# Optimization experiments

Hardware: AMD Instinct MI355X
Metric: run time of the kernel (lower is better)

## Reference

```python
import jax, jax.numpy as jnp
import numpy as np

EXP_SCALE = 10.0   # self.exp_param_scale
BETA_UP = 5.0      # self.kernel_beta_upbound
N_HEAD = 12


def setup_inputs() -> dict:
    key = jax.random.key(0)
    ks = jax.random.split(key, 7)
    B, T, C, nh = 2, 2048, 768, N_HEAD
    s = 1.0 / np.sqrt(C)
    x = jax.random.normal(ks[0], (B, T, C), jnp.float32)
    W_la = jax.random.normal(ks[1], (C, C), jnp.float32) * s      # LeakyAverage linear
    la_coef = jax.random.uniform(ks[2], (nh,), jnp.float32)        # per-head leaky decay in (0,1)
    W_v = jax.random.normal(ks[3], (C, C), jnp.float32) * s        # v_featurizer linear
    v_coef = jax.random.uniform(ks[4], (nh,), jnp.float32)         # v_featurizer per-head coef
    kernel_beta = jnp.ones((nh,), jnp.float32) / EXP_SCALE
    value_beta = jnp.ones((nh,), jnp.float32) * (-0.5 / EXP_SCALE)
    W_proj = jax.random.normal(ks[5], (C, C), jnp.float32) * s     # c_proj
    return dict(x=x, W_la=W_la, la_coef=la_coef, W_v=W_v, v_coef=v_coef,
                kernel_beta=kernel_beta, value_beta=value_beta, W_proj=W_proj)


def _leaky_average(x, W_la, la_coef):
    # y_t = c * y_{t-1} + (1-c) * (x W^T)_t, per-head decay c. Returns (B, nh, T, hs).
    B, T, C = x.shape
    nh = la_coef.shape[0]
    hs = C // nh
    u = (x @ W_la.T).reshape(B, T, nh, hs)
    c = la_coef[None, :, None]  # (1, nh, 1) broadcast over (B, nh, hs)

    def step(carry, ut):
        y = c * carry + (1.0 - c) * ut
        return y, y

    _, ys = jax.lax.scan(step, jnp.zeros((B, nh, hs), x.dtype), jnp.swapaxes(u, 0, 1))
    return jnp.transpose(ys, (1, 2, 0, 3))  # (T,B,nh,hs) -> (B,nh,T,hs)


def reference(x, W_la, la_coef, W_v, v_coef, kernel_beta, value_beta, W_proj):
    B, T, C = x.shape
    nh = la_coef.shape[0]
    hs = C // nh
    v_shift = 1

    # K path: leaky-average features, L2-normalize, exp-kernel beta scale
    k0 = _leaky_average(x, W_la, la_coef)                               # (B,nh,T,hs)
    raw_k = k0 / (jnp.linalg.norm(k0, axis=-1, keepdims=True) + 1e-6)
    beta = jnp.exp(jnp.minimum(kernel_beta * EXP_SCALE, BETA_UP))
    k = raw_k * beta[None, :, None, None]

    # V path: lowrlinearconv featurizer (linear, shift-by-1 mix, normalize) + value scale
    xl = (x @ W_v.T).reshape(B, T, nh, hs).transpose(0, 2, 1, 3)        # (B,nh,T,hs)
    shifted = jnp.concatenate([xl[:, :, 1:], jnp.zeros_like(xl[:, :, :1])], axis=2)
    vc = v_coef[None, :, None, None]
    vf = shifted * (1.0 - vc) + xl * vc
    vf = vf / (jnp.linalg.norm(vf, axis=-1, keepdims=True) + 1e-6)
    vbeta = jnp.exp(jnp.minimum(value_beta * EXP_SCALE, BETA_UP))
    v = vf * vbeta[None, :, None, None]

    # shifted-causal attention: query at position t (t>=1) attends keys 0..t-1, scale=1.0
    q = k[:, :, v_shift:]                                               # (B,nh,T-1,hs)
    scores = jnp.einsum('bhqd,bhkd->bhqk', q, k)                        # (B,nh,T-1,T)
    mask = jnp.tril(jnp.ones((T - v_shift, T), bool))                   # j <= iq  <=>  key < query pos
    scores = jnp.where(mask, scores, -jnp.inf)
    attn = jax.nn.softmax(scores, axis=-1)
    o = jnp.einsum('bhqk,bhkd->bhqd', attn, v)
    y = jnp.concatenate([jnp.zeros((B, nh, v_shift, hs), x.dtype), o], axis=2)

    y = y.transpose(0, 2, 1, 3).reshape(B, T, C)
    return y @ W_proj.T  # c_proj (dropouts are identity in eval)
```

## Files before the change

kernel.cpp:

```cpp
#include <hip/hip_runtime.h>
#include <hip/hip_bf16.h>
#include <math.h>

#define B_   2
#define T_   2048
#define C_   768
#define NH   12
#define HS   64
#define NSEG 64
#define SEGLEN 32
#define CX   1536

typedef __attribute__((ext_vector_type(8))) short short8;
typedef __attribute__((ext_vector_type(4))) short short4v;
typedef __attribute__((ext_vector_type(4))) float f32x4;

static __device__ inline unsigned short f2b(float f) {
  __hip_bfloat16 h = __float2bfloat16(f);
  unsigned short u;
  __builtin_memcpy(&u, &h, 2);
  return u;
}
static __device__ inline float b2f(unsigned short u) {
  unsigned int x = ((unsigned int)u) << 16;
  float f;
  __builtin_memcpy(&f, &x, 4);
  return f;
}

#define GLOAD_LDS16(gp, lp)                                                        \
  __builtin_amdgcn_global_load_lds((const __attribute__((address_space(1))) void*)(gp), \
                                   (__attribute__((address_space(3))) void*)(lp), 16, 0, 0)

__global__ __launch_bounds__(256) void cast_all(const float* __restrict__ x,
                                                const float* __restrict__ wla,
                                                const float* __restrict__ wv,
                                                const float* __restrict__ wp,
                                                __hip_bfloat16* __restrict__ xb,
                                                __hip_bfloat16* __restrict__ wcat,
                                                __hip_bfloat16* __restrict__ wpb) {
  const int NX4 = (B_ * T_ * C_) / 4;
  const int NW4 = (C_ * C_) / 4;
  const int TOT = NX4 + 3 * NW4;
  int i = blockIdx.x * 256 + threadIdx.x;
  int st = gridDim.x * 256;
  for (; i < TOT; i += st) {
    const float* s;
    unsigned short* d;
    if (i < NX4) { s = x + (size_t)i * 4; d = (unsigned short*)xb + (size_t)i * 4; }
    else if (i < NX4 + NW4) { int j = i - NX4; s = wla + (size_t)j * 4; d = (unsigned short*)wcat + (size_t)j * 4; }
    else if (i < NX4 + 2 * NW4) { int j = i - NX4 - NW4; s = wv + (size_t)j * 4; d = (unsigned short*)wcat + (size_t)(C_ * C_) + (size_t)j * 4; }
    else { int j = i - NX4 - 2 * NW4; s = wp + (size_t)j * 4; d = (unsigned short*)wpb + (size_t)j * 4; }
    float4 v = *(const float4*)s;
    short4v o;
    o.x = (short)f2b(v.x); o.y = (short)f2b(v.y); o.z = (short)f2b(v.z); o.w = (short)f2b(v.w);
    *(short4v*)d = o;
  }
}

template <int BM, bool OB16>
__global__ __launch_bounds__(256) void gemm_bf16(const __hip_bfloat16* __restrict__ A,
                                                 const __hip_bfloat16* __restrict__ Bw,
                                                 void* __restrict__ Cv,
                                                 int M, int N, int K) {
  __shared__ __hip_bfloat16 As[BM * 64];
  __shared__ __hip_bfloat16 Bs[128 * 64];
  const int tid = threadIdx.x;
  const int w = tid >> 6, lane = tid & 63;
  const int bm = blockIdx.x * BM, bn = blockIdx.y * 128;
  const int q16 = lane & 15, lg = lane >> 4;

  constexpr int NACC = (BM == 128) ? 4 : 2;
  f32x4 acc[4][NACC];
#pragma unroll
  for (int i = 0; i < 4; ++i)
#pragma unroll
    for (int j = 0; j < NACC; ++j) acc[i][j] = (f32x4){0.f, 0.f, 0.f, 0.f};

  const int srow = (lane >> 3);
  const int soff0 = (lane & 7) * 16;
  const int sw = (lane & 7) << 4;
  constexpr int ACH = BM / 8;
  constexpr int CPW = (ACH + 16) / 4;

  for (int k0 = 0; k0 < K; k0 += 64) {
    __syncthreads();
#pragma unroll
    for (int c = 0; c < CPW; ++c) {
      int gc = w * CPW + c;
      int isB = gc >= ACH;
      int ci = isB ? gc - ACH : gc;
      int row = ci * 8 + srow;
      int soff = soff0 ^ ((row & 7) << 4);
      const __hip_bfloat16* gp =
          (isB ? Bw + (size_t)(bn + row) * K : A + (size_t)(bm + row) * K) + k0 + (soff >> 1);
      __hip_bfloat16* lp = (isB ? Bs : As) + ci * 512;
      GLOAD_LDS16(gp, lp);
    }
    __syncthreads();
#pragma unroll
    for (int ks = 0; ks < 2; ++ks) {
      short8 af[4], bf[NACC];
      const int colb = ks * 64 + lg * 16;
#pragma unroll
      for (int i = 0; i < 4; ++i) {
        int ra = (BM == 128) ? ((w >> 1) * 64 + i * 16 + q16) : (i * 16 + q16);
        af[i] = *(const short8*)((const char*)As + ra * 128 + (colb ^ sw));
      }
#pragma unroll
      for (int j = 0; j < NACC; ++j) {
        int rb = (BM == 128) ? ((w & 1) * 64 + j * 16 + q16) : (w * 32 + j * 16 + q16);
        bf[j] = *(const short8*)((const char*)Bs + rb * 128 + (colb ^ sw));
      }
#pragma unroll
      for (int i = 0; i < 4; ++i)
#pragma unroll
        for (int j = 0; j < NACC; ++j)
          acc[i][j] = __builtin_amdgcn_mfma_f32_16x16x32_bf16(af[i], bf[j], acc[i][j], 0, 0, 0);
    }
  }
#pragma unroll
  for (int i = 0; i < 4; ++i) {
#pragma unroll
    for (int r = 0; r < 4; ++r) {
      int m = (BM == 128) ? (bm + (w >> 1) * 64 + i * 16 + lg * 4 + r)
                          : (bm + i * 16 + lg * 4 + r);
      int nb = (BM == 128) ? (bn + (w & 1) * 64 + q16) : (bn + w * 32 + q16);
      if (OB16) {
        unsigned short* cp = (unsigned short*)Cv + (size_t)m * N + nb;
#pragma unroll
        for (int j = 0; j < NACC; ++j) cp[j * 16] = f2b(acc[i][j][r]);
      } else {
        float* cp = (float*)Cv + (size_t)m * N + nb;
#pragma unroll
        for (int j = 0; j < NACC; ++j) cp[j * 16] = acc[i][j][r];
      }
    }
  }
}

__global__ __launch_bounds__(256) void scan_seg(const unsigned short* __restrict__ uxv,
                                                const float* __restrict__ la_coef,
                                                float* __restrict__ segend) {
  int cid = blockIdx.x * 4 + (threadIdx.x >> 6);
  int d   = threadIdx.x & 63;
  int seg = cid & (NSEG - 1);
  int bh  = cid >> 6;
  int h   = bh % NH;
  int b   = bh / NH;
  float c  = la_coef[h];
  float oc = 1.f - c;
  int t0 = seg * SEGLEN;
  const unsigned short* up = uxv + ((size_t)b * T_ + t0) * CX + h * HS + d;
  float uv[SEGLEN];
#pragma unroll
  for (int i = 0; i < SEGLEN; ++i) uv[i] = b2f(up[(size_t)i * CX]);
  float y = 0.f;
#pragma unroll
  for (int i = 0; i < SEGLEN; ++i) y = fmaf(c, y, oc * uv[i]);
  segend[(size_t)cid * HS + d] = y;
}

__global__ __launch_bounds__(256) void scan_b(const float* __restrict__ la_coef,
                                              const float* __restrict__ segend,
                                              float* __restrict__ carryin) {
  int s = blockIdx.x * 256 + threadIdx.x;
  if (s >= B_ * NH * HS) return;
  int d  = s & 63;
  int bh = s >> 6;
  int h  = bh % NH;
  float c = la_coef[h];
  float cl = c;
#pragma unroll
  for (int i = 0; i < 5; ++i) cl *= cl;
  float h0 = 0.f;
  for (int seg = 0; seg < NSEG; ++seg) {
    int cid = bh * NSEG + seg;
    carryin[(size_t)cid * HS + d] = h0;
    h0 = fmaf(cl, h0, segend[(size_t)cid * HS + d]);
  }
}

__global__ __launch_bounds__(256) void scanc_vbuild(const float* __restrict__ la_coef,
                                                    const float* __restrict__ kernel_beta,
                                                    const float* __restrict__ carryin,
                                                    const unsigned short* __restrict__ uxv,
                                                    const float* __restrict__ v_coef,
                                                    const float* __restrict__ value_beta,
                                                    __hip_bfloat16* __restrict__ kb16,
                                                    __hip_bfloat16* __restrict__ vt) {
  __shared__ __hip_bfloat16 sm[64][73];
  const int NBC = B_ * NH * NSEG / 4;
  if ((int)blockIdx.x < NBC) {
    int cid = blockIdx.x * 4 + (threadIdx.x >> 6);
    int d   = threadIdx.x & 63;
    int seg = cid & (NSEG - 1);
    int bh  = cid >> 6;
    int h   = bh % NH;
    int b   = bh / NH;
    float c  = la_coef[h];
    float oc = 1.f - c;
    float bk = __expf(fminf(kernel_beta[h] * 10.f, 5.f));
    int t0 = seg * SEGLEN;
    const unsigned short* up = uxv + ((size_t)b * T_ + t0) * CX + h * HS + d;
    __hip_bfloat16* op = kb16 + ((size_t)bh * T_ + t0) * HS + d;
    float uv[SEGLEN];
#pragma unroll
    for (int i = 0; i < SEGLEN; ++i) uv[i] = b2f(up[(size_t)i * CX]);
    float y = carryin[(size_t)cid * HS + d];
    for (int i = 0; i < SEGLEN; ++i) {
      y = fmaf(c, y, oc * uv[i]);
      float ss = y * y;
#pragma unroll
      for (int off = 1; off < 64; off <<= 1) ss += __shfl_xor(ss, off, 64);
      float scale = bk / (sqrtf(ss) + 1e-6f);
      op[(size_t)i * HS] = __float2bfloat16(y * scale);
    }
  } else {
    int idx = blockIdx.x - NBC;
    int t0 = (idx & 31) * 64;
    int bh = idx >> 5;
    int h = bh % NH, b = bh / NH;
    int w = threadIdx.x >> 6, lane = threadIdx.x & 63;
    float vc = v_coef[h];
    float vb = __expf(fminf(value_beta[h] * 10.f, 5.f));
    for (int i = 0; i < 16; ++i) {
      int tl = w * 16 + i;
      int t = t0 + tl;
      const unsigned short* xp = uxv + ((size_t)b * T_ + t) * CX + 768 + h * HS + lane;
      float x0 = b2f(*xp);
      float x1 = (t + 1 < T_) ? b2f(xp[CX]) : 0.f;
      float vf = (1.f - vc) * x1 + vc * x0;
      float ss = vf * vf;
#pragma unroll
      for (int off = 1; off < 64; off <<= 1) ss += __shfl_xor(ss, off, 64);
      sm[tl][lane] = __float2bfloat16(vf * vb / (sqrtf(ss) + 1e-6f));
    }
    __syncthreads();
    int d = threadIdx.x >> 3;
    int c = threadIdx.x & 7;
    for (int i = 0; i < 2; ++i) {
      int dd = d + i * 32;
      short8 v;
#pragma unroll
      for (int k = 0; k < 8; ++k)
        v[k] = (short)((const unsigned short*)&sm[c * 8 + k][dd])[0];
      *(short8*)((unsigned short*)vt + ((size_t)bh * HS + dd) * T_ + t0 + c * 8) = v;
    }
  }
}

__global__ __launch_bounds__(256, 4) void attn7(const __hip_bfloat16* __restrict__ Kg,
                                                const __hip_bfloat16* __restrict__ Vtg,
                                                const float* __restrict__ kernel_beta,
                                                __hip_bfloat16* __restrict__ Y) {
  __shared__ __hip_bfloat16 Kt[2][64 * 64];
  __shared__ __hip_bfloat16 Vt[3][64 * 64];
  __shared__ char Pl[4][2304];
  const int bh = blockIdx.x;
  const int b = bh / NH, h = bh % NH;
  const int w = threadIdx.x >> 6, lane = threadIdx.x & 63;
  const int q16 = lane & 15, lg = lane >> 4;
  const int it = 31 - blockIdx.y;
  const int qb0 = 1 + it * 64;
  float bk = __expf(fminf(kernel_beta[h] * 10.f, 5.f));
  const float L2E = 1.4426950408889634f;
  float m0l = bk * bk * L2E;
  const unsigned short* Kh = (const unsigned short*)Kg + (size_t)bh * T_ * HS;
  const unsigned short* Vh = (const unsigned short*)Vtg + (size_t)bh * HS * T_;
  unsigned short* Yh = (unsigned short*)Y + (size_t)b * T_ * C_ + h * HS;

  if (it == 0 && w == 0) Yh[lane] = 0;

  const int tq = qb0 + w * 16 + q16;
  short8 qf[2];
  {
    int tqc = tq > T_ - 1 ? T_ - 1 : tq;
#pragma unroll
    for (int ks = 0; ks < 2; ++ks)
      qf[ks] = *(const short8*)(Kh + (size_t)tqc * HS + ks * 32 + lg * 8);
  }

  f32x4 zero = {0.f, 0.f, 0.f, 0.f};
  f32x4 accO[4];
#pragma unroll
  for (int mt = 0; mt < 4; ++mt) accO[mt] = zero;
  float lsum = 0.f;
  f32x4 sp[4];

  char* pb = &Pl[w][0] + q16 * 144;
  const int swr = (q16 & 7) << 4;

  const int srow = lane >> 3;
  const int soff = ((lane & 7) << 4) ^ (srow << 4);

  const int NT = (qb0 + 126) >> 6;

#define STAGE_KV(kbuf, vbuf, j0)                                                      \
  {                                                                                   \
    _Pragma("unroll")                                                                 \
    for (int n = 0; n < 2; ++n) {                                                     \
      int ch = w * 2 + n;                                                             \
      int row = ch * 8 + srow;                                                        \
      GLOAD_LDS16((const char*)(Kh + (size_t)((j0) + row) * HS) + soff,               \
                  &Kt[kbuf][ch * 512]);                                               \
      GLOAD_LDS16((const char*)(Vh + (size_t)row * T_ + (j0)) + soff,                 \
                  &Vt[vbuf][ch * 512]);                                               \
    }                                                                                 \
  }

#define SM_PV(tp)                                                                     \
  {                                                                                   \
    const int j0p = (tp)*64;                                                          \
    const char* Vb = (const char*)&Vt[(tp) % 3][0];                                   \
    _Pragma("unroll")                                                                 \
    for (int nt = 0; nt < 4; ++nt) {                                                  \
      float p[4];                                                                     \
      _Pragma("unroll")                                                               \
      for (int r = 0; r < 4; ++r) {                                                   \
        int j = j0p + nt * 16 + lg * 4 + r;                                           \
        p[r] = (j < tq) ? exp2f(fmaf(sp[nt][r], L2E, -m0l)) : 0.f;                    \
        lsum += p[r];                                                                 \
      }                                                                               \
      unsigned int w0, w1;                                                            \
      asm("v_cvt_pk_bf16_f32 %0, %1, %2" : "=v"(w0) : "v"(p[0]), "v"(p[1]));          \
      asm("v_cvt_pk_bf16_f32 %0, %1, %2" : "=v"(w1) : "v"(p[2]), "v"(p[3]));          \
      uint2 pk; pk.x = w0; pk.y = w1;                                                 \
      *(uint2*)(pb + nt * 32 + lg * 8) = pk;                                          \
    }                                                                                 \
    __builtin_amdgcn_s_setprio(1);                                                    \
    _Pragma("unroll")                                                                 \
    for (int ks = 0; ks < 2; ++ks) {                                                  \
      short8 pf = *(const short8*)(pb + ks * 64 + lg * 16);                           \
      _Pragma("unroll")                                                               \
      for (int mt = 0; mt < 4; ++mt) {                                                \
        short8 vf = *(const short8*)(Vb + (mt * 16 + q16) * 128 +                     \
                                     ((ks * 64 + lg * 16) ^ swr));                    \
        accO[mt] = __builtin_amdgcn_mfma_f32_16x16x32_bf16(vf, pf, accO[mt], 0, 0, 0);\
      }                                                                               \
    }                                                                                 \
    __builtin_amdgcn_s_setprio(0);                                                    \
  }

  STAGE_KV(0, 0, 0);

  for (int kt = 0; kt < NT; ++kt) {
    const int j0 = kt * 64;
    if (kt + 1 < NT) {
      STAGE_KV((kt + 1) & 1, (kt + 1) % 3, j0 + 64);
      asm volatile("s_waitcnt vmcnt(4)" ::: "memory");
    } else {
      asm volatile("s_waitcnt vmcnt(0)" ::: "memory");
    }
    __builtin_amdgcn_s_barrier();
    __builtin_amdgcn_sched_barrier(0);

    const char* Kb = (const char*)&Kt[kt & 1][0];
    short8 kf[4][2];
#pragma unroll
    for (int nt = 0; nt < 4; ++nt)
#pragma unroll
      for (int ks = 0; ks < 2; ++ks)
        kf[nt][ks] = *(const short8*)(Kb + (nt * 16 + q16) * 128 + ((ks * 64 + lg * 16) ^ swr));
    f32x4 sc[4];
    __builtin_amdgcn_s_setprio(1);
#pragma unroll
    for (int nt = 0; nt < 4; ++nt) {
      sc[nt] = __builtin_amdgcn_mfma_f32_16x16x32_bf16(kf[nt][0], qf[0], zero, 0, 0, 0);
      sc[nt] = __builtin_amdgcn_mfma_f32_16x16x32_bf16(kf[nt][1], qf[1], sc[nt], 0, 0, 0);
    }
    __builtin_amdgcn_s_setprio(0);

    if (kt > 0) SM_PV(kt - 1);

#pragma unroll
    for (int nt = 0; nt < 4; ++nt) sp[nt] = sc[nt];

    asm volatile("s_waitcnt lgkmcnt(0)" ::: "memory");
    __builtin_amdgcn_s_barrier();
  }
  SM_PV(NT - 1);

  {
    float v = lsum;
    v += __shfl_xor(v, 16, 64);
    v += __shfl_xor(v, 32, 64);
    float inv = 1.f / v;
    if (tq < T_) {
      unsigned short* yp = Yh + (size_t)tq * C_;
#pragma unroll
      for (int mt = 0; mt < 4; ++mt) {
        float o0 = accO[mt][0] * inv, o1 = accO[mt][1] * inv;
        float o2 = accO[mt][2] * inv, o3 = accO[mt][3] * inv;
        unsigned int u0, u1;
        asm("v_cvt_pk_bf16_f32 %0, %1, %2" : "=v"(u0) : "v"(o0), "v"(o1));
        asm("v_cvt_pk_bf16_f32 %0, %1, %2" : "=v"(u1) : "v"(o2), "v"(o3));
        uint2 pk; pk.x = u0; pk.y = u1;
        *(uint2*)(yp + mt * 16 + lg * 4) = pk;
      }
    }
  }
#undef STAGE_KV
#undef SM_PV
}

extern "C" void kernel_launch(void* const* d_in, const int* in_sizes, int n_in,
                              void* d_out, int out_size, void* d_ws, size_t ws_size,
                              hipStream_t stream) {
  const float* x          = (const float*)d_in[0];
  const float* W_la       = (const float*)d_in[1];
  const float* la_coef    = (const float*)d_in[2];
  const float* W_v        = (const float*)d_in[3];
  const float* v_coef     = (const float*)d_in[4];
  const float* kernel_bet = (const float*)d_in[5];
  const float* value_bet  = (const float*)d_in[6];
  const float* W_proj     = (const float*)d_in[7];
  float* out = (float*)d_out;

  char* ws = (char*)d_ws;
  const size_t NTOK = (size_t)B_ * T_ * C_;
  const size_t NSEGTOT = (size_t)B_ * NH * NSEG * HS;
  unsigned short* uxv = (unsigned short*)ws;
  float* segend  = (float*)(ws + (size_t)B_ * T_ * CX * 2);
  float* carryin = segend + NSEGTOT;
  __hip_bfloat16* kb16 = (__hip_bfloat16*)(carryin + NSEGTOT);
  __hip_bfloat16* vt16 = kb16 + NTOK;
  __hip_bfloat16* xb   = vt16 + NTOK;
  __hip_bfloat16* Wcat = xb + NTOK;
  __hip_bfloat16* Wpb  = Wcat + (size_t)CX * C_;
  __hip_bfloat16* yb   = xb;

  const int M = B_ * T_;

  cast_all<<<2048, 256, 0, stream>>>(x, W_la, W_v, W_proj, xb, Wcat, Wpb);

  gemm_bf16<64, true><<<dim3(M / 64, CX / 128), 256, 0, stream>>>(xb, Wcat, uxv, M, CX, C_);

  scan_seg<<<dim3(B_ * NH * NSEG / 4), 256, 0, stream>>>(uxv, la_coef, segend);
  scan_b<<<dim3((B_ * NH * HS + 255) / 256), 256, 0, stream>>>(la_coef, segend, carryin);
  scanc_vbuild<<<dim3(B_ * NH * NSEG / 4 + 32 * B_ * NH), 256, 0, stream>>>(
      la_coef, kernel_bet, carryin, uxv, v_coef, value_bet, kb16, vt16);

  attn7<<<dim3(B_ * NH, 32), 256, 0, stream>>>(kb16, vt16, kernel_bet, yb);

  gemm_bf16<64, false><<<dim3(M / 64, C_ / 128), 256, 0, stream>>>(yb, Wpb, out, M, C_, C_);
}
```

Measured before the change: 104.4 us.

## Split attention keys across waves and fold carry scan into consumer kernel

The attention kernel now has each of the four waves handle all 64 queries of the block but only a strided quarter of the 32-key tiles. K/V fragments are loaded straight from global into registers with double buffering, and partial outputs and row sums are reduced through LDS at the end, replacing the shared-LDS staging, barriers and query-per-wave split. Separately, the scan_b kernel is removed and each segment recomputes its carry-in by serially combining the preceding segment ends. This saves a launch but adds up to 63 dependent FMAs per thread. The attention change raises register pressure (launch bounds lowered to 2) and drops LDS reuse of K/V across waves.

```diff
diff --git a/kernel.cpp b/kernel.cpp
--- a/kernel.cpp
+++ b/kernel.cpp
@@ -161,29 +161,9 @@
   segend[(size_t)cid * HS + d] = y;
 }
 
-__global__ __launch_bounds__(256) void scan_b(const float* __restrict__ la_coef,
-                                              const float* __restrict__ segend,
-                                              float* __restrict__ carryin) {
-  int s = blockIdx.x * 256 + threadIdx.x;
-  if (s >= B_ * NH * HS) return;
-  int d  = s & 63;
-  int bh = s >> 6;
-  int h  = bh % NH;
-  float c = la_coef[h];
-  float cl = c;
-#pragma unroll
-  for (int i = 0; i < 5; ++i) cl *= cl;
-  float h0 = 0.f;
-  for (int seg = 0; seg < NSEG; ++seg) {
-    int cid = bh * NSEG + seg;
-    carryin[(size_t)cid * HS + d] = h0;
-    h0 = fmaf(cl, h0, segend[(size_t)cid * HS + d]);
-  }
-}
-
 __global__ __launch_bounds__(256) void scanc_vbuild(const float* __restrict__ la_coef,
                                                     const float* __restrict__ kernel_beta,
-                                                    const float* __restrict__ carryin,
+                                                    const float* __restrict__ segend,
                                                     const unsigned short* __restrict__ uxv,
                                                     const float* __restrict__ v_coef,
                                                     const float* __restrict__ value_beta,
@@ -201,13 +181,18 @@
     float c  = la_coef[h];
     float oc = 1.f - c;
     float bk = __expf(fminf(kernel_beta[h] * 10.f, 5.f));
+    float cl = c;
+#pragma unroll
+    for (int i = 0; i < 5; ++i) cl *= cl;
+    const float* se = segend + (size_t)bh * NSEG * HS + d;
+    float y = 0.f;
+    for (int s = 0; s < seg; ++s) y = fmaf(y, cl, se[(size_t)s * HS]);
     int t0 = seg * SEGLEN;
     const unsigned short* up = uxv + ((size_t)b * T_ + t0) * CX + h * HS + d;
     __hip_bfloat16* op = kb16 + ((size_t)bh * T_ + t0) * HS + d;
     float uv[SEGLEN];
 #pragma unroll
     for (int i = 0; i < SEGLEN; ++i) uv[i] = b2f(up[(size_t)i * CX]);
-    float y = carryin[(size_t)cid * HS + d];
     for (int i = 0; i < SEGLEN; ++i) {
       y = fmaf(c, y, oc * uv[i]);
       float ss = y * y;
@@ -250,158 +235,176 @@
   }
 }
 
-__global__ __launch_bounds__(256, 4) void attn7(const __hip_bfloat16* __restrict__ Kg,
+__global__ __launch_bounds__(256, 2) void attn8(const __hip_bfloat16* __restrict__ Kg,
                                                 const __hip_bfloat16* __restrict__ Vtg,
                                                 const float* __restrict__ kernel_beta,
                                                 __hip_bfloat16* __restrict__ Y) {
-  __shared__ __hip_bfloat16 Kt[2][64 * 64];
-  __shared__ __hip_bfloat16 Vt[3][64 * 64];
-  __shared__ char Pl[4][2304];
+  __shared__ __align__(16) char lds[38912];
   const int bh = blockIdx.x;
   const int b = bh / NH, h = bh % NH;
   const int w = threadIdx.x >> 6, lane = threadIdx.x & 63;
   const int q16 = lane & 15, lg = lane >> 4;
   const int it = 31 - blockIdx.y;
   const int qb0 = 1 + it * 64;
+  const int NT32 = 2 * it + 2;
   float bk = __expf(fminf(kernel_beta[h] * 10.f, 5.f));
   const float L2E = 1.4426950408889634f;
-  float m0l = bk * bk * L2E;
+  const float m0l = bk * bk * L2E;
   const unsigned short* Kh = (const unsigned short*)Kg + (size_t)bh * T_ * HS;
   const unsigned short* Vh = (const unsigned short*)Vtg + (size_t)bh * HS * T_;
   unsigned short* Yh = (unsigned short*)Y + (size_t)b * T_ * C_ + h * HS;
 
   if (it == 0 && w == 0) Yh[lane] = 0;
 
-  const int tq = qb0 + w * 16 + q16;
-  short8 qf[2];
-  {
-    int tqc = tq > T_ - 1 ? T_ - 1 : tq;
+  short8 qf[4][2];
+#pragma unroll
+  for (int qs = 0; qs < 4; ++qs) {
+    int tqc = qb0 + qs * 16 + q16;
+    if (tqc > T_ - 1) tqc = T_ - 1;
 #pragma unroll
     for (int ks = 0; ks < 2; ++ks)
-      qf[ks] = *(const short8*)(Kh + (size_t)tqc * HS + ks * 32 + lg * 8);
+      qf[qs][ks] = *(const short8*)(Kh + (size_t)tqc * HS + ks * 32 + lg * 8);
   }
 
   f32x4 zero = {0.f, 0.f, 0.f, 0.f};
-  f32x4 accO[4];
-#pragma unroll
-  for (int mt = 0; mt < 4; ++mt) accO[mt] = zero;
-  float lsum = 0.f;
-  f32x4 sp[4];
-
-  char* pb = &Pl[w][0] + q16 * 144;
-  const int swr = (q16 & 7) << 4;
-
-  const int srow = lane >> 3;
-  const int soff = ((lane & 7) << 4) ^ (srow << 4);
-
-  const int NT = (qb0 + 126) >> 6;
-
-#define STAGE_KV(kbuf, vbuf, j0)                                                      \
+  f32x4 accO[4][4];
+#pragma unroll
+  for (int qs = 0; qs < 4; ++qs)
+#pragma unroll
+    for (int mt = 0; mt < 4; ++mt) accO[qs][mt] = zero;
+  float lsum[4] = {0.f, 0.f, 0.f, 0.f};
+  char* pwbase = lds + (size_t)w * 4 * 1152;
+
+#define LOADT(KF, VF, j0)                                                             \
   {                                                                                   \
     _Pragma("unroll")                                                                 \
-    for (int n = 0; n < 2; ++n) {                                                     \
-      int ch = w * 2 + n;                                                             \
-      int row = ch * 8 + srow;                                                        \
-      GLOAD_LDS16((const char*)(Kh + (size_t)((j0) + row) * HS) + soff,               \
-                  &Kt[kbuf][ch * 512]);                                               \
-      GLOAD_LDS16((const char*)(Vh + (size_t)row * T_ + (j0)) + soff,                 \
-                  &Vt[vbuf][ch * 512]);                                               \
-    }                                                                                 \
-  }
-
-#define SM_PV(tp)                                                                     \
+    for (int nt = 0; nt < 2; ++nt)                                                    \
+      _Pragma("unroll")                                                               \
+      for (int ks = 0; ks < 2; ++ks)                                                  \
+        KF[nt][ks] = *(const short8*)(Kh + (size_t)((j0) + nt * 16 + q16) * HS +      \
+                                      ks * 32 + lg * 8);                              \
+    _Pragma("unroll")                                                                 \
+    for (int mt = 0; mt < 4; ++mt)                                                    \
+      VF[mt] = *(const short8*)(Vh + (size_t)(mt * 16 + q16) * T_ + (j0) + lg * 8);   \
+  }
+
+#define COMPUTE(KF, VF, ktv)                                                          \
   {                                                                                   \
-    const int j0p = (tp)*64;                                                          \
-    const char* Vb = (const char*)&Vt[(tp) % 3][0];                                   \
+    const int j0c = (ktv)*32;                                                         \
     _Pragma("unroll")                                                                 \
-    for (int nt = 0; nt < 4; ++nt) {                                                  \
-      float p[4];                                                                     \
+    for (int qs = 0; qs < 4; ++qs) {                                                  \
+      const int tqq = qb0 + qs * 16 + q16;                                            \
+      char* pb = pwbase + qs * 1152 + q16 * 72;                                       \
+      f32x4 s0 = __builtin_amdgcn_mfma_f32_16x16x32_bf16(KF[0][0], qf[qs][0], zero, 0, 0, 0); \
+      s0 = __builtin_amdgcn_mfma_f32_16x16x32_bf16(KF[0][1], qf[qs][1], s0, 0, 0, 0); \
+      f32x4 s1 = __builtin_amdgcn_mfma_f32_16x16x32_bf16(KF[1][0], qf[qs][0], zero, 0, 0, 0); \
+      s1 = __builtin_amdgcn_mfma_f32_16x16x32_bf16(KF[1][1], qf[qs][1], s1, 0, 0, 0); \
+      float p0[4], p1[4];                                                             \
       _Pragma("unroll")                                                               \
       for (int r = 0; r < 4; ++r) {                                                   \
-        int j = j0p + nt * 16 + lg * 4 + r;                                           \
-        p[r] = (j < tq) ? exp2f(fmaf(sp[nt][r], L2E, -m0l)) : 0.f;                    \
-        lsum += p[r];                                                                 \
+        int j0r = j0c + lg * 4 + r;                                                   \
+        p0[r] = (j0r < tqq) ? exp2f(fmaf(s0[r], L2E, -m0l)) : 0.f;                    \
+        int j1r = j0c + 16 + lg * 4 + r;                                              \
+        p1[r] = (j1r < tqq) ? exp2f(fmaf(s1[r], L2E, -m0l)) : 0.f;                    \
+        lsum[qs] += p0[r] + p1[r];                                                    \
       }                                                                               \
-      unsigned int w0, w1;                                                            \
-      asm("v_cvt_pk_bf16_f32 %0, %1, %2" : "=v"(w0) : "v"(p[0]), "v"(p[1]));          \
-      asm("v_cvt_pk_bf16_f32 %0, %1, %2" : "=v"(w1) : "v"(p[2]), "v"(p[3]));          \
-      uint2 pk; pk.x = w0; pk.y = w1;                                                 \
-      *(uint2*)(pb + nt * 32 + lg * 8) = pk;                                          \
+      unsigned int w00, w01, w10, w11;                                                \
+      asm("v_cvt_pk_bf16_f32 %0, %1, %2" : "=v"(w00) : "v"(p0[0]), "v"(p0[1]));       \
+      asm("v_cvt_pk_bf16_f32 %0, %1, %2" : "=v"(w01) : "v"(p0[2]), "v"(p0[3]));       \
+      asm("v_cvt_pk_bf16_f32 %0, %1, %2" : "=v"(w10) : "v"(p1[0]), "v"(p1[1]));       \
+      asm("v_cvt_pk_bf16_f32 %0, %1, %2" : "=v"(w11) : "v"(p1[2]), "v"(p1[3]));       \
+      uint2 pkA; pkA.x = w00; pkA.y = w01;                                            \
+      uint2 pkB; pkB.x = w10; pkB.y = w11;                                            \
+      *(uint2*)(pb + lg * 8) = pkA;                                                   \
+      *(uint2*)(pb + 32 + lg * 8) = pkB;                                              \
+      short8 pf = *(const short8*)(pb + lg * 16);                                     \
+      _Pragma("unroll")                                                               \
+      for (int mt = 0; mt < 4; ++mt)                                                  \
+        accO[qs][mt] = __builtin_amdgcn_mfma_f32_16x16x32_bf16(VF[mt], pf, accO[qs][mt], 0, 0, 0); \
     }                                                                                 \
-    __builtin_amdgcn_s_setprio(1);                                                    \
-    _Pragma("unroll")                                                                 \
-    for (int ks = 0; ks < 2; ++ks) {                                                  \
-      short8 pf = *(const short8*)(pb + ks * 64 + lg * 16);                           \
-      _Pragma("unroll")                                                               \
-      for (int mt = 0; mt < 4; ++mt) {                                                \
-        short8 vf = *(const short8*)(Vb + (mt * 16 + q16) * 128 +                     \
-                                     ((ks * 64 + lg * 16) ^ swr));                    \
-        accO[mt] = __builtin_amdgcn_mfma_f32_16x16x32_bf16(vf, pf, accO[mt], 0, 0, 0);\
-      }                                                                               \
-    }                                                                                 \
-    __builtin_amdgcn_s_setprio(0);                                                    \
-  }
-
-  STAGE_KV(0, 0, 0);
-
-  for (int kt = 0; kt < NT; ++kt) {
-    const int j0 = kt * 64;
-    if (kt + 1 < NT) {
-      STAGE_KV((kt + 1) & 1, (kt + 1) % 3, j0 + 64);
-      asm volatile("s_waitcnt vmcnt(4)" ::: "memory");
-    } else {
-      asm volatile("s_waitcnt vmcnt(0)" ::: "memory");
-    }
-    __builtin_amdgcn_s_barrier();
-    __builtin_amdgcn_sched_barrier(0);
-
-    const char* Kb = (const char*)&Kt[kt & 1][0];
-    short8 kf[4][2];
-#pragma unroll
-    for (int nt = 0; nt < 4; ++nt)
-#pragma unroll
-      for (int ks = 0; ks < 2; ++ks)
-        kf[nt][ks] = *(const short8*)(Kb + (nt * 16 + q16) * 128 + ((ks * 64 + lg * 16) ^ swr));
-    f32x4 sc[4];
-    __builtin_amdgcn_s_setprio(1);
-#pragma unroll
-    for (int nt = 0; nt < 4; ++nt) {
-      sc[nt] = __builtin_amdgcn_mfma_f32_16x16x32_bf16(kf[nt][0], qf[0], zero, 0, 0, 0);
-      sc[nt] = __builtin_amdgcn_mfma_f32_16x16x32_bf16(kf[nt][1], qf[1], sc[nt], 0, 0, 0);
-    }
-    __builtin_amdgcn_s_setprio(0);
-
-    if (kt > 0) SM_PV(kt - 1);
-
-#pragma unroll
-    for (int nt = 0; nt < 4; ++nt) sp[nt] = sc[nt];
-
-    asm volatile("s_waitcnt lgkmcnt(0)" ::: "memory");
-    __builtin_amdgcn_s_barrier();
-  }
-  SM_PV(NT - 1);
-
-  {
-    float v = lsum;
-    v += __shfl_xor(v, 16, 64);
-    v += __shfl_xor(v, 32, 64);
-    float inv = 1.f / v;
-    if (tq < T_) {
-      unsigned short* yp = Yh + (size_t)tq * C_;
+  }
+
+  short8 kfA[2][2], vfA[4], kfB[2][2], vfB[4];
+  int kt = w;
+  if (kt < NT32) LOADT(kfA, vfA, kt * 32);
+  while (kt < NT32) {
+    if (kt + 4 < NT32) LOADT(kfB, vfB, (kt + 4) * 32);
+    COMPUTE(kfA, vfA, kt);
+    kt += 4;
+    if (kt >= NT32) break;
+    if (kt + 4 < NT32) LOADT(kfA, vfA, (kt + 4) * 32);
+    COMPUTE(kfB, vfB, kt);
+    kt += 4;
+  }
+
+  __syncthreads();
+  float* LR = (float*)(lds + 34816);
+  if (w >= 2) {
+    float* PB = (float*)(lds + (size_t)(w - 2) * 17408);
+#pragma unroll
+    for (int qs = 0; qs < 4; ++qs)
+#pragma unroll
+      for (int mt = 0; mt < 4; ++mt)
+        *(f32x4*)(PB + (qs * 16 + q16) * 68 + mt * 16 + lg * 4) = accO[qs][mt];
+  }
+#pragma unroll
+  for (int qs = 0; qs < 4; ++qs)
+    LR[((size_t)w * 64 + qs * 16 + q16) * 4 + lg] = lsum[qs];
+  __syncthreads();
+  if (w < 2) {
+    float* PB = (float*)(lds + (size_t)w * 17408);
+#pragma unroll
+    for (int qs = 0; qs < 4; ++qs)
 #pragma unroll
       for (int mt = 0; mt < 4; ++mt) {
-        float o0 = accO[mt][0] * inv, o1 = accO[mt][1] * inv;
-        float o2 = accO[mt][2] * inv, o3 = accO[mt][3] * inv;
-        unsigned int u0, u1;
-        asm("v_cvt_pk_bf16_f32 %0, %1, %2" : "=v"(u0) : "v"(o0), "v"(o1));
-        asm("v_cvt_pk_bf16_f32 %0, %1, %2" : "=v"(u1) : "v"(o2), "v"(o3));
-        uint2 pk; pk.x = u0; pk.y = u1;
-        *(uint2*)(yp + mt * 16 + lg * 4) = pk;
-      }
-    }
-  }
-#undef STAGE_KV
-#undef SM_PV
+        f32x4 o = *(f32x4*)(PB + (qs * 16 + q16) * 68 + mt * 16 + lg * 4);
+        accO[qs][mt][0] += o[0]; accO[qs][mt][1] += o[1];
+        accO[qs][mt][2] += o[2]; accO[qs][mt][3] += o[3];
+      }
+    if (w == 1) {
+#pragma unroll
+      for (int qs = 0; qs < 4; ++qs)
+#pragma unroll
+        for (int mt = 0; mt < 4; ++mt)
+          *(f32x4*)(PB + (qs * 16 + q16) * 68 + mt * 16 + lg * 4) = accO[qs][mt];
+    }
+  }
+  __syncthreads();
+  if (w == 0) {
+    float* PB1 = (float*)(lds + 17408);
+#pragma unroll
+    for (int qs = 0; qs < 4; ++qs) {
+#pragma unroll
+      for (int mt = 0; mt < 4; ++mt) {
+        f32x4 o = *(f32x4*)(PB1 + (qs * 16 + q16) * 68 + mt * 16 + lg * 4);
+        accO[qs][mt][0] += o[0]; accO[qs][mt][1] += o[1];
+        accO[qs][mt][2] += o[2]; accO[qs][mt][3] += o[3];
+      }
+      float tot = 0.f;
+#pragma unroll
+      for (int p = 0; p < 4; ++p) {
+        f32x4 lv = *(f32x4*)(LR + ((size_t)p * 64 + qs * 16 + q16) * 4);
+        tot += lv[0] + lv[1] + lv[2] + lv[3];
+      }
+      float inv = 1.f / tot;
+      int tq = qb0 + qs * 16 + q16;
+      if (tq < T_) {
+        unsigned short* yp = Yh + (size_t)tq * C_;
+#pragma unroll
+        for (int mt = 0; mt < 4; ++mt) {
+          float o0 = accO[qs][mt][0] * inv, o1 = accO[qs][mt][1] * inv;
+          float o2 = accO[qs][mt][2] * inv, o3 = accO[qs][mt][3] * inv;
+          unsigned int u0, u1;
+          asm("v_cvt_pk_bf16_f32 %0, %1, %2" : "=v"(u0) : "v"(o0), "v"(o1));
+          asm("v_cvt_pk_bf16_f32 %0, %1, %2" : "=v"(u1) : "v"(o2), "v"(o3));
+          uint2 pk; pk.x = u0; pk.y = u1;
+          *(uint2*)(yp + mt * 16 + lg * 4) = pk;
+        }
+      }
+    }
+  }
+#undef LOADT
+#undef COMPUTE
 }
 
 extern "C" void kernel_launch(void* const* d_in, const int* in_sizes, int n_in,
@@ -422,8 +425,7 @@
   const size_t NSEGTOT = (size_t)B_ * NH * NSEG * HS;
   unsigned short* uxv = (unsigned short*)ws;
   float* segend  = (float*)(ws + (size_t)B_ * T_ * CX * 2);
-  float* carryin = segend + NSEGTOT;
-  __hip_bfloat16* kb16 = (__hip_bfloat16*)(carryin + NSEGTOT);
+  __hip_bfloat16* kb16 = (__hip_bfloat16*)(segend + NSEGTOT);
   __hip_bfloat16* vt16 = kb16 + NTOK;
   __hip_bfloat16* xb   = vt16 + NTOK;
   __hip_bfloat16* Wcat = xb + NTOK;
@@ -437,11 +439,10 @@
   gemm_bf16<64, true><<<dim3(M / 64, CX / 128), 256, 0, stream>>>(xb, Wcat, uxv, M, CX, C_);
 
   scan_seg<<<dim3(B_ * NH * NSEG / 4), 256, 0, stream>>>(uxv, la_coef, segend);
-  scan_b<<<dim3((B_ * NH * HS + 255) / 256), 256, 0, stream>>>(la_coef, segend, carryin);
   scanc_vbuild<<<dim3(B_ * NH * NSEG / 4 + 32 * B_ * NH), 256, 0, stream>>>(
-      la_coef, kernel_bet, carryin, uxv, v_coef, value_bet, kb16, vt16);
-
-  attn7<<<dim3(B_ * NH, 32), 256, 0, stream>>>(kb16, vt16, kernel_bet, yb);
+      la_coef, kernel_bet, segend, uxv, v_coef, value_bet, kb16, vt16);
+
+  attn8<<<dim3(B_ * NH, 32), 256, 0, stream>>>(kb16, vt16, kernel_bet, yb);
 
   gemm_bf16<64, false><<<dim3(M / 64, C_ / 128), 256, 0, stream>>>(yb, Wpb, out, M, C_, C_);
 }
```

After: 110.3 us. +5.7%, slower.

## Rewrite attention as split-K 32x32 MFMA with paired query tiles and register P

Applied to the files above, without the earlier changes.

Replaces the attention kernel with one where each block handles two 32-row query tiles (p and 63-p) for causal load balancing. The four waves split the key range, each loading K and V tiles directly from global into registers and using 32x32x16 MFMAs. The P fragment is repacked with permlane32_swap instead of going through LDS, and partial outputs are reduced across waves through LDS at the end. Separately, the carry scan preloads segment ends into registers. The aim is to cut LDS traffic and barriers, at the cost of a cross-wave reduction and higher register pressure (launch bounds drop to 2).

```diff
diff --git a/kernel.cpp b/kernel.cpp
--- a/kernel.cpp
+++ b/kernel.cpp
@@ -14,6 +14,9 @@
 typedef __attribute__((ext_vector_type(8))) short short8;
 typedef __attribute__((ext_vector_type(4))) short short4v;
 typedef __attribute__((ext_vector_type(4))) float f32x4;
+typedef __attribute__((ext_vector_type(16))) float f32x16;
+typedef __attribute__((ext_vector_type(2))) unsigned int uint2v;
+typedef __attribute__((ext_vector_type(4))) unsigned int uint4v;
 
 static __device__ inline unsigned short f2b(float f) {
   __hip_bfloat16 h = __float2bfloat16(f);
@@ -26,6 +29,11 @@
   float f;
   __builtin_memcpy(&f, &x, 4);
   return f;
+}
+static __device__ inline unsigned cvtpk(float a, float b) {
+  unsigned r;
+  asm("v_cvt_pk_bf16_f32 %0, %1, %2" : "=v"(r) : "v"(a), "v"(b));
+  return r;
 }
 
 #define GLOAD_LDS16(gp, lp)                                                        \
@@ -173,11 +181,15 @@
   float cl = c;
 #pragma unroll
   for (int i = 0; i < 5; ++i) cl *= cl;
+  float sv[NSEG];
+#pragma unroll
+  for (int seg = 0; seg < NSEG; ++seg)
+    sv[seg] = segend[(size_t)(bh * NSEG + seg) * HS + d];
   float h0 = 0.f;
+#pragma unroll
   for (int seg = 0; seg < NSEG; ++seg) {
-    int cid = bh * NSEG + seg;
-    carryin[(size_t)cid * HS + d] = h0;
-    h0 = fmaf(cl, h0, segend[(size_t)cid * HS + d]);
+    carryin[(size_t)(bh * NSEG + seg) * HS + d] = h0;
+    h0 = fmaf(cl, h0, sv[seg]);
   }
 }
 
@@ -250,158 +262,226 @@
   }
 }
 
-__global__ __launch_bounds__(256, 4) void attn7(const __hip_bfloat16* __restrict__ Kg,
-                                                const __hip_bfloat16* __restrict__ Vtg,
-                                                const float* __restrict__ kernel_beta,
-                                                __hip_bfloat16* __restrict__ Y) {
-  __shared__ __hip_bfloat16 Kt[2][64 * 64];
-  __shared__ __hip_bfloat16 Vt[3][64 * 64];
-  __shared__ char Pl[4][2304];
+__global__ __launch_bounds__(256, 2) void attn12(const __hip_bfloat16* __restrict__ Kg,
+                                                 const __hip_bfloat16* __restrict__ Vtg,
+                                                 const float* __restrict__ kernel_beta,
+                                                 __hip_bfloat16* __restrict__ Y) {
+  __shared__ __align__(16) char lds[20992];
   const int bh = blockIdx.x;
   const int b = bh / NH, h = bh % NH;
   const int w = threadIdx.x >> 6, lane = threadIdx.x & 63;
-  const int q16 = lane & 15, lg = lane >> 4;
-  const int it = 31 - blockIdx.y;
-  const int qb0 = 1 + it * 64;
+  const int l31 = lane & 31, lg2 = lane >> 5;
+  const int p = blockIdx.y;
+  const int uA = p, uB = 63 - p;
   float bk = __expf(fminf(kernel_beta[h] * 10.f, 5.f));
   const float L2E = 1.4426950408889634f;
-  float m0l = bk * bk * L2E;
+  const float m0l = bk * bk * L2E;
   const unsigned short* Kh = (const unsigned short*)Kg + (size_t)bh * T_ * HS;
   const unsigned short* Vh = (const unsigned short*)Vtg + (size_t)bh * HS * T_;
   unsigned short* Yh = (unsigned short*)Y + (size_t)b * T_ * C_ + h * HS;
 
-  if (it == 0 && w == 0) Yh[lane] = 0;
-
-  const int tq = qb0 + w * 16 + q16;
-  short8 qf[2];
+  if (p == 0 && w == 0) Yh[lane] = 0;
+
+  short8 qfA[4], qfB[4];
   {
-    int tqc = tq > T_ - 1 ? T_ - 1 : tq;
-#pragma unroll
-    for (int ks = 0; ks < 2; ++ks)
-      qf[ks] = *(const short8*)(Kh + (size_t)tqc * HS + ks * 32 + lg * 8);
-  }
-
-  f32x4 zero = {0.f, 0.f, 0.f, 0.f};
-  f32x4 accO[4];
-#pragma unroll
-  for (int mt = 0; mt < 4; ++mt) accO[mt] = zero;
-  float lsum = 0.f;
-  f32x4 sp[4];
-
-  char* pb = &Pl[w][0] + q16 * 144;
-  const int swr = (q16 & 7) << 4;
-
-  const int srow = lane >> 3;
-  const int soff = ((lane & 7) << 4) ^ (srow << 4);
-
-  const int NT = (qb0 + 126) >> 6;
-
-#define STAGE_KV(kbuf, vbuf, j0)                                                      \
+    int ta = 1 + 32 * uA + l31; if (ta > T_ - 1) ta = T_ - 1;
+    int tb = 1 + 32 * uB + l31; if (tb > T_ - 1) tb = T_ - 1;
+#pragma unroll
+    for (int s = 0; s < 4; ++s) {
+      qfA[s] = *(const short8*)(Kh + (size_t)ta * HS + s * 16 + lg2 * 8);
+      qfB[s] = *(const short8*)(Kh + (size_t)tb * HS + s * 16 + lg2 * 8);
+    }
+  }
+
+  f32x16 zero16 = {0.f};
+  f32x16 accA[2] = {zero16, zero16}, accB[2] = {zero16, zero16};
+  float lsA = 0.f, lsB = 0.f;
+
+#define LOADT(KF, VF, j0)                                                             \
   {                                                                                   \
     _Pragma("unroll")                                                                 \
-    for (int n = 0; n < 2; ++n) {                                                     \
-      int ch = w * 2 + n;                                                             \
-      int row = ch * 8 + srow;                                                        \
-      GLOAD_LDS16((const char*)(Kh + (size_t)((j0) + row) * HS) + soff,               \
-                  &Kt[kbuf][ch * 512]);                                               \
-      GLOAD_LDS16((const char*)(Vh + (size_t)row * T_ + (j0)) + soff,                 \
-                  &Vt[vbuf][ch * 512]);                                               \
-    }                                                                                 \
-  }
-
-#define SM_PV(tp)                                                                     \
+    for (int s = 0; s < 4; ++s)                                                       \
+      KF[s] = *(const short8*)(Kh + (size_t)((j0) + l31) * HS + s * 16 + lg2 * 8);    \
+    _Pragma("unroll")                                                                 \
+    for (int ds = 0; ds < 2; ++ds)                                                    \
+      _Pragma("unroll")                                                               \
+      for (int s2 = 0; s2 < 2; ++s2)                                                  \
+        VF[ds][s2] = *(const short8*)(Vh + (size_t)(ds * 32 + l31) * T_ + (j0) +      \
+                                      s2 * 16 + lg2 * 8);                             \
+  }
+
+#define PACK_P(pq)                                                                    \
+  uint2v g00 = __builtin_amdgcn_permlane32_swap(cvtpk(pq[0], pq[1]),                  \
+                                                cvtpk(pq[4], pq[5]), false, false);   \
+  uint2v g01 = __builtin_amdgcn_permlane32_swap(cvtpk(pq[2], pq[3]),                  \
+                                                cvtpk(pq[6], pq[7]), false, false);   \
+  uint2v g10 = __builtin_amdgcn_permlane32_swap(cvtpk(pq[8], pq[9]),                  \
+                                                cvtpk(pq[12], pq[13]), false, false); \
+  uint2v g11 = __builtin_amdgcn_permlane32_swap(cvtpk(pq[10], pq[11]),                \
+                                                cvtpk(pq[14], pq[15]), false, false); \
+  uint4v pb0v, pb1v;                                                                  \
+  pb0v.x = g00.x; pb0v.y = g01.x; pb0v.z = g00.y; pb0v.w = g01.y;                     \
+  pb1v.x = g10.x; pb1v.y = g11.x; pb1v.z = g10.y; pb1v.w = g11.y;                     \
+  short8 PB0 = __builtin_bit_cast(short8, pb0v);                                      \
+  short8 PB1 = __builtin_bit_cast(short8, pb1v);
+
+#define PV_STEP(VF, ACC)                                                              \
   {                                                                                   \
-    const int j0p = (tp)*64;                                                          \
-    const char* Vb = (const char*)&Vt[(tp) % 3][0];                                   \
-    _Pragma("unroll")                                                                 \
-    for (int nt = 0; nt < 4; ++nt) {                                                  \
-      float p[4];                                                                     \
+    __builtin_amdgcn_s_setprio(1);                                                    \
+    _Pragma("unroll")                                                                 \
+    for (int ds = 0; ds < 2; ++ds) {                                                  \
+      ACC[ds] = __builtin_amdgcn_mfma_f32_32x32x16_bf16(VF[ds][0], PB0, ACC[ds], 0, 0, 0); \
+      ACC[ds] = __builtin_amdgcn_mfma_f32_32x32x16_bf16(VF[ds][1], PB1, ACC[ds], 0, 0, 0); \
+    }                                                                                 \
+    __builtin_amdgcn_s_setprio(0);                                                    \
+  }
+
+#define COMPUTE_U(KF, VF, QF, ACC, LSUM)                                              \
+  {                                                                                   \
+    f32x16 S = zero16;                                                                \
+    __builtin_amdgcn_s_setprio(1);                                                    \
+    _Pragma("unroll")                                                                 \
+    for (int s = 0; s < 4; ++s)                                                       \
+      S = __builtin_amdgcn_mfma_f32_32x32x16_bf16(KF[s], QF[s], S, 0, 0, 0);          \
+    __builtin_amdgcn_s_setprio(0);                                                    \
+    float pq[16];                                                                     \
+    _Pragma("unroll")                                                                 \
+    for (int r = 0; r < 16; ++r) {                                                    \
+      pq[r] = exp2f(fmaf(S[r], L2E, -m0l));                                           \
+      LSUM += pq[r];                                                                  \
+    }                                                                                 \
+    PACK_P(pq);                                                                       \
+    PV_STEP(VF, ACC);                                                                 \
+  }
+
+#define COMPUTE_M(KF, VF, ktv, QF, ACC, LSUM, ULO)                                    \
+  {                                                                                   \
+    const int jb = (ktv)*32 + 4 * lg2;                                                \
+    const int tqq = (ULO) + l31;                                                      \
+    f32x16 S = zero16;                                                                \
+    _Pragma("unroll")                                                                 \
+    for (int s = 0; s < 4; ++s)                                                       \
+      S = __builtin_amdgcn_mfma_f32_32x32x16_bf16(KF[s], QF[s], S, 0, 0, 0);          \
+    float pq[16];                                                                     \
+    _Pragma("unroll")                                                                 \
+    for (int r = 0; r < 16; ++r) {                                                    \
+      int jg = jb + (r & 3) + 8 * (r >> 2);                                           \
+      pq[r] = (jg < tqq) ? exp2f(fmaf(S[r], L2E, -m0l)) : 0.f;                        \
+      LSUM += pq[r];                                                                  \
+    }                                                                                 \
+    PACK_P(pq);                                                                       \
+    PV_STEP(VF, ACC);                                                                 \
+  }
+
+#define DO_UNIT(QF, ACC, LSUM, LIM, ULO)                                              \
+  {                                                                                   \
+    int kt = w;                                                                       \
+    short8 kfa[4], vfa[2][2], kfb[4], vfb[2][2];                                      \
+    if (kt < (LIM)) {                                                                 \
+      LOADT(kfa, vfa, kt * 32);                                                       \
+      while (true) {                                                                  \
+        if (kt + 4 < (LIM)) LOADT(kfb, vfb, (kt + 4) * 32);                           \
+        COMPUTE_U(kfa, vfa, QF, ACC, LSUM);                                           \
+        kt += 4;                                                                      \
+        if (kt >= (LIM)) break;                                                       \
+        if (kt + 4 < (LIM)) LOADT(kfa, vfa, (kt + 4) * 32);                           \
+        COMPUTE_U(kfb, vfb, QF, ACC, LSUM);                                           \
+        kt += 4;                                                                      \
+        if (kt >= (LIM)) break;                                                       \
+      }                                                                               \
+    }                                                                                 \
+    for (; kt <= (LIM); kt += 4) {                                                    \
+      LOADT(kfa, vfa, kt * 32);                                                       \
+      COMPUTE_M(kfa, vfa, kt, QF, ACC, LSUM, ULO);                                    \
+    }                                                                                 \
+  }
+
+  DO_UNIT(qfA, accA, lsA, uA, 1 + 32 * uA);
+  DO_UNIT(qfB, accB, lsB, uB, 1 + 32 * uB);
+
+  lsA += __shfl_xor(lsA, 32, 64);
+  lsB += __shfl_xor(lsB, 32, 64);
+
+#define COMBINE(ACC, LS, U)                                                           \
+  {                                                                                   \
+    float* LR = (float*)(lds + 20480);                                                \
+    __syncthreads();                                                                  \
+    if (w >= 2) {                                                                     \
+      float* PB = (float*)(lds + (size_t)(w - 2) * 10240);                            \
       _Pragma("unroll")                                                               \
-      for (int r = 0; r < 4; ++r) {                                                   \
-        int j = j0p + nt * 16 + lg * 4 + r;                                           \
-        p[r] = (j < tq) ? exp2f(fmaf(sp[nt][r], L2E, -m0l)) : 0.f;                    \
-        lsum += p[r];                                                                 \
+      for (int ds = 0; ds < 2; ++ds) {                                                \
+        float* rb = PB + (ds * 64 + lane) * 20;                                       \
+        _Pragma("unroll")                                                             \
+        for (int c = 0; c < 4; ++c)                                                   \
+          *(f32x4*)(rb + c * 4) = (f32x4){ACC[ds][c * 4 + 0], ACC[ds][c * 4 + 1],     \
+                                          ACC[ds][c * 4 + 2], ACC[ds][c * 4 + 3]};    \
       }                                                                               \
-      unsigned int w0, w1;                                                            \
-      asm("v_cvt_pk_bf16_f32 %0, %1, %2" : "=v"(w0) : "v"(p[0]), "v"(p[1]));          \
-      asm("v_cvt_pk_bf16_f32 %0, %1, %2" : "=v"(w1) : "v"(p[2]), "v"(p[3]));          \
-      uint2 pk; pk.x = w0; pk.y = w1;                                                 \
-      *(uint2*)(pb + nt * 32 + lg * 8) = pk;                                          \
-    }                                                                                 \
-    __builtin_amdgcn_s_setprio(1);                                                    \
-    _Pragma("unroll")                                                                 \
-    for (int ks = 0; ks < 2; ++ks) {                                                  \
-      short8 pf = *(const short8*)(pb + ks * 64 + lg * 16);                           \
+    }                                                                                 \
+    LR[w * 32 + l31] = LS;                                                            \
+    __syncthreads();                                                                  \
+    if (w < 2) {                                                                      \
+      float* PB = (float*)(lds + (size_t)w * 10240);                                  \
       _Pragma("unroll")                                                               \
-      for (int mt = 0; mt < 4; ++mt) {                                                \
-        short8 vf = *(const short8*)(Vb + (mt * 16 + q16) * 128 +                     \
-                                     ((ks * 64 + lg * 16) ^ swr));                    \
-        accO[mt] = __builtin_amdgcn_mfma_f32_16x16x32_bf16(vf, pf, accO[mt], 0, 0, 0);\
+      for (int ds = 0; ds < 2; ++ds) {                                                \
+        float* rb = PB + (ds * 64 + lane) * 20;                                       \
+        _Pragma("unroll")                                                             \
+        for (int c = 0; c < 4; ++c) {                                                 \
+          f32x4 o = *(f32x4*)(rb + c * 4);                                            \
+          ACC[ds][c * 4 + 0] += o[0]; ACC[ds][c * 4 + 1] += o[1];                     \
+          ACC[ds][c * 4 + 2] += o[2]; ACC[ds][c * 4 + 3] += o[3];                     \
+        }                                                                             \
       }                                                                               \
-    }                                                                                 \
-    __builtin_amdgcn_s_setprio(0);                                                    \
-  }
-
-  STAGE_KV(0, 0, 0);
-
-  for (int kt = 0; kt < NT; ++kt) {
-    const int j0 = kt * 64;
-    if (kt + 1 < NT) {
-      STAGE_KV((kt + 1) & 1, (kt + 1) % 3, j0 + 64);
-      asm volatile("s_waitcnt vmcnt(4)" ::: "memory");
-    } else {
-      asm volatile("s_waitcnt vmcnt(0)" ::: "memory");
-    }
-    __builtin_amdgcn_s_barrier();
-    __builtin_amdgcn_sched_barrier(0);
-
-    const char* Kb = (const char*)&Kt[kt & 1][0];
-    short8 kf[4][2];
-#pragma unroll
-    for (int nt = 0; nt < 4; ++nt)
-#pragma unroll
-      for (int ks = 0; ks < 2; ++ks)
-        kf[nt][ks] = *(const short8*)(Kb + (nt * 16 + q16) * 128 + ((ks * 64 + lg * 16) ^ swr));
-    f32x4 sc[4];
-    __builtin_amdgcn_s_setprio(1);
-#pragma unroll
-    for (int nt = 0; nt < 4; ++nt) {
-      sc[nt] = __builtin_amdgcn_mfma_f32_16x16x32_bf16(kf[nt][0], qf[0], zero, 0, 0, 0);
-      sc[nt] = __builtin_amdgcn_mfma_f32_16x16x32_bf16(kf[nt][1], qf[1], sc[nt], 0, 0, 0);
-    }
-    __builtin_amdgcn_s_setprio(0);
-
-    if (kt > 0) SM_PV(kt - 1);
-
-#pragma unroll
-    for (int nt = 0; nt < 4; ++nt) sp[nt] = sc[nt];
-
-    asm volatile("s_waitcnt lgkmcnt(0)" ::: "memory");
-    __builtin_amdgcn_s_barrier();
-  }
-  SM_PV(NT - 1);
-
-  {
-    float v = lsum;
-    v += __shfl_xor(v, 16, 64);
-    v += __shfl_xor(v, 32, 64);
-    float inv = 1.f / v;
-    if (tq < T_) {
-      unsigned short* yp = Yh + (size_t)tq * C_;
-#pragma unroll
-      for (int mt = 0; mt < 4; ++mt) {
-        float o0 = accO[mt][0] * inv, o1 = accO[mt][1] * inv;
-        float o2 = accO[mt][2] * inv, o3 = accO[mt][3] * inv;
-        unsigned int u0, u1;
-        asm("v_cvt_pk_bf16_f32 %0, %1, %2" : "=v"(u0) : "v"(o0), "v"(o1));
-        asm("v_cvt_pk_bf16_f32 %0, %1, %2" : "=v"(u1) : "v"(o2), "v"(o3));
-        uint2 pk; pk.x = u0; pk.y = u1;
-        *(uint2*)(yp + mt * 16 + lg * 4) = pk;
-      }
-    }
-  }
-#undef STAGE_KV
-#undef SM_PV
+      if (w == 1) {                                                                   \
+        _Pragma("unroll")                                                             \
+        for (int ds = 0; ds < 2; ++ds) {                                              \
+          float* rb = PB + (ds * 64 + lane) * 20;                                     \
+          _Pragma("unroll")                                                           \
+          for (int c = 0; c < 4; ++c)                                                 \
+            *(f32x4*)(rb + c * 4) = (f32x4){ACC[ds][c * 4 + 0], ACC[ds][c * 4 + 1],   \
+                                            ACC[ds][c * 4 + 2], ACC[ds][c * 4 + 3]};  \
+        }                                                                             \
+      }                                                                               \
+    }                                                                                 \
+    __syncthreads();                                                                  \
+    if (w == 0) {                                                                     \
+      float* PB1 = (float*)(lds + 10240);                                             \
+      _Pragma("unroll")                                                               \
+      for (int ds = 0; ds < 2; ++ds) {                                                \
+        float* rb = PB1 + (ds * 64 + lane) * 20;                                      \
+        _Pragma("unroll")                                                             \
+        for (int c = 0; c < 4; ++c) {                                                 \
+          f32x4 o = *(f32x4*)(rb + c * 4);                                            \
+          ACC[ds][c * 4 + 0] += o[0]; ACC[ds][c * 4 + 1] += o[1];                     \
+          ACC[ds][c * 4 + 2] += o[2]; ACC[ds][c * 4 + 3] += o[3];                     \
+        }                                                                             \
+      }                                                                               \
+      float tot = LR[0 * 32 + l31] + LR[1 * 32 + l31] +                               \
+                  LR[2 * 32 + l31] + LR[3 * 32 + l31];                                \
+      float inv = 1.f / tot;                                                          \
+      int tq = 1 + 32 * (U) + l31;                                                    \
+      if (tq < T_) {                                                                  \
+        unsigned short* yp = Yh + (size_t)tq * C_;                                    \
+        _Pragma("unroll")                                                             \
+        for (int ds = 0; ds < 2; ++ds)                                                \
+          _Pragma("unroll")                                                           \
+          for (int r = 0; r < 16; r += 2) {                                           \
+            int dd = ds * 32 + (r & 3) + 8 * (r >> 2) + 4 * lg2;                      \
+            unsigned u2 = cvtpk(ACC[ds][r] * inv, ACC[ds][r + 1] * inv);              \
+            *(unsigned*)(yp + dd) = u2;                                               \
+          }                                                                           \
+      }                                                                               \
+    }                                                                                 \
+  }
+
+  COMBINE(accA, lsA, uA);
+  COMBINE(accB, lsB, uB);
+#undef LOADT
+#undef PACK_P
+#undef PV_STEP
+#undef COMPUTE_U
+#undef COMPUTE_M
+#undef DO_UNIT
+#undef COMBINE
 }
 
 extern "C" void kernel_launch(void* const* d_in, const int* in_sizes, int n_in,
@@ -441,7 +521,7 @@
   scanc_vbuild<<<dim3(B_ * NH * NSEG / 4 + 32 * B_ * NH), 256, 0, stream>>>(
       la_coef, kernel_bet, carryin, uxv, v_coef, value_bet, kb16, vt16);
 
-  attn7<<<dim3(B_ * NH, 32), 256, 0, stream>>>(kb16, vt16, kernel_bet, yb);
+  attn12<<<dim3(B_ * NH, 32), 256, 0, stream>>>(kb16, vt16, kernel_bet, yb);
 
   gemm_bf16<64, false><<<dim3(M / 64, C_ / 128), 256, 0, stream>>>(yb, Wpb, out, M, C_, C_);
 }
```

New measurement: 111.6 us. 6.9% more time.
